# Kernel tuning notes

Measured on AMD Instinct MI355X. Metric: run time of the kernel, lower is better.

## Reference

```python
import jax, jax.numpy as jnp
import numpy as np

# Module constants (from init_kwargs)
D_MODEL = 2048
N_HEAD = 16
D_HEAD = D_MODEL // N_HEAD  # 128
CH = N_HEAD + D_HEAD        # 144
R_Q, R_K, R_V = 6, 2, 2
ROPE_BASE = 10000.0
B, T = 2, 2048


def _rotary(b, cache_len):
    # b: [B, T, R, dh]; rotary applied in factor space, positions offset by cache_len
    dh = b.shape[-1]
    inv_freq = (1.0 / ROPE_BASE) ** (jnp.arange(0, dh, 2, dtype=jnp.float32) / dh)
    t = jnp.arange(b.shape[1], dtype=jnp.float32) + cache_len
    freqs = t[:, None] * inv_freq[None, :]             # [T, dh/2]
    cos = jnp.cos(freqs)[None, :, None, :]
    sin = jnp.sin(freqs)[None, :, None, :]
    x1, x2 = jnp.split(b, 2, axis=-1)
    y1 = x1 * cos + x2 * sin
    y2 = -x1 * sin + x2 * cos
    return jnp.concatenate([y1, y2], axis=-1).astype(b.dtype)


def setup_inputs() -> dict:
    key = jax.random.key(0)
    k0, k1, k2, k3 = jax.random.split(key, 4)
    s = 1.0 / np.sqrt(D_MODEL)
    return {
        "x": jax.random.normal(k0, (B, T, D_MODEL), dtype=jnp.float32),
        "W_q": jax.random.normal(k1, (R_Q * CH, D_MODEL), dtype=jnp.float32) * s,
        "W_kv": jax.random.normal(k2, ((R_K + R_V) * CH, D_MODEL), dtype=jnp.float32) * s,
        "W_o": jax.random.normal(k3, (D_MODEL, D_MODEL), dtype=jnp.float32) * s,
    }


def reference(x, W_q, W_kv, W_o):
    Bx, Tx, D = x.shape
    nh, dh = N_HEAD, D_HEAD
    cache_len = 0  # empty cache, full prefill

    # Factorized Q projection: [B,T,r_Q,ch]
    abq = (x @ W_q.T).reshape(Bx, Tx, R_Q, CH)
    a_q, b_q = abq[..., :nh], abq[..., nh:]

    # Factorized KV projection, rotary in factor space on the b-part
    abkv = (x @ W_kv.T).reshape(Bx, Tx, R_K + R_V, CH)
    a_kv = abkv[..., :nh]
    b_kv = _rotary(abkv[..., nh:], cache_len)

    a_k, b_k = a_kv[:, :, :R_K], b_kv[:, :, :R_K]
    a_v, b_v = a_kv[:, :, R_K:], b_kv[:, :, R_K:]

    # Rank-r outer-product reconstruction: [B,T,nh,dh]
    q = jnp.einsum("btrh,btrd->bthd", a_q, b_q) * (1.0 / R_Q)
    k = jnp.einsum("btrh,btrd->bthd", a_k, b_k) * (1.0 / R_K)
    v = jnp.einsum("btrh,btrd->bthd", a_v, b_v) * (1.0 / R_V)

    # Causal attention (flex_attention default scale = 1/sqrt(dh))
    scale = 1.0 / np.sqrt(dh)
    scores = jnp.einsum("bqhd,bkhd->bhqk", q, k) * scale
    qi = jnp.arange(Tx)[:, None]
    ki = jnp.arange(Tx)[None, :]
    causal = ki <= qi + cache_len
    scores = jnp.where(causal[None, None], scores, jnp.finfo(scores.dtype).min)
    attn = jax.nn.softmax(scores, axis=-1)
    y = jnp.einsum("bhqk,bkhd->bqhd", attn, v).reshape(Bx, Tx, D)
    return y @ W_o.T
```

## Files before the change

kernel.cpp:

```cpp
#include <hip/hip_runtime.h>
#include <hip/hip_bf16.h>
#include <cstdint>
#include <cstddef>

#define T_SEQ   2048
#define BATCH   2
#define DMODEL  2048
#define NHEAD   16
#define DHEAD   128
#define CH      144
#define RQ      6
#define RKV     4
#define N1      1440
#define N1P     1536
#define MROWS   4096

typedef short bf16x8 __attribute__((ext_vector_type(8)));
typedef float f32x4  __attribute__((ext_vector_type(4)));

#if defined(__has_builtin)
#  if __has_builtin(__builtin_amdgcn_exp2f)
#    define EXP2(x) __builtin_amdgcn_exp2f(x)
#  else
#    define EXP2(x) exp2f(x)
#  endif
#else
#  define EXP2(x) exp2f(x)
#endif

__device__ __forceinline__ float bflo(unsigned u){ return __uint_as_float(u << 16); }
__device__ __forceinline__ float bfhi(unsigned u){ return __uint_as_float(u & 0xffff0000u); }
__device__ __forceinline__ unsigned short f2bf(float f){
  unsigned b = __float_as_uint(f);
  b += 0x7fffu + ((b >> 16) & 1u);
  return (unsigned short)(b >> 16);
}

__global__ void cast_f32_bf16(const float* __restrict__ src, unsigned short* __restrict__ dst, int n4){
  int i = blockIdx.x * blockDim.x + threadIdx.x;
  int stride = gridDim.x * blockDim.x;
  for (; i < n4; i += stride){
    float4 v = ((const float4*)src)[i];
    ushort4 o;
    o.x = f2bf(v.x); o.y = f2bf(v.y); o.z = f2bf(v.z); o.w = f2bf(v.w);
    ((ushort4*)dst)[i] = o;
  }
}

__global__ void zero_u16(unsigned short* __restrict__ dst, int n){
  int i = blockIdx.x * blockDim.x + threadIdx.x;
  if (i < n) dst[i] = 0;
}

#define GBK 32
__global__ __launch_bounds__(256) void gemm_bt(const unsigned short* __restrict__ A,
                                               const unsigned short* __restrict__ Bm,
                                               float* __restrict__ C,
                                               int M, int N, int K){
  __shared__ __align__(16) unsigned short As[128 * GBK];
  __shared__ __align__(16) unsigned short Bs[128 * GBK];
  const int tid  = threadIdx.x;
  const int lane = tid & 63;
  const int wv   = tid >> 6;
  const int m0   = blockIdx.y * 128;
  const int n0   = blockIdx.x * 128;
  const int wm   = wv >> 1, wn = wv & 1;

  f32x4 acc[4][4];
#pragma unroll
  for (int i = 0; i < 4; ++i)
#pragma unroll
    for (int j = 0; j < 4; ++j) acc[i][j] = (f32x4){0.f, 0.f, 0.f, 0.f};

  const int srow = lane >> 2;
  const int scol = (lane & 3) * 8;
  const int kq   = (lane >> 4) * 8;
  const int rA   = lane & 15;

  for (int kt = 0; kt < K; kt += GBK){
#pragma unroll
    for (int i = 0; i < 2; ++i){
      int j = wv * 2 + i;
      int r = j * 16 + srow;
      const unsigned short* ga = A  + (size_t)(m0 + r) * K + kt + scol;
      const unsigned short* gb = Bm + (size_t)(n0 + r) * K + kt + scol;
      __builtin_amdgcn_global_load_lds((const __attribute__((address_space(1))) void*)ga,
                                       (__attribute__((address_space(3))) void*)&As[j * 16 * GBK], 16, 0, 0);
      __builtin_amdgcn_global_load_lds((const __attribute__((address_space(1))) void*)gb,
                                       (__attribute__((address_space(3))) void*)&Bs[j * 16 * GBK], 16, 0, 0);
    }
    __syncthreads();

    bf16x8 af[4], bfv[4];
#pragma unroll
    for (int mi = 0; mi < 4; ++mi)
      af[mi] = *(const bf16x8*)&As[(wm * 64 + mi * 16 + rA) * GBK + kq];
#pragma unroll
    for (int ni = 0; ni < 4; ++ni)
      bfv[ni] = *(const bf16x8*)&Bs[(wn * 64 + ni * 16 + rA) * GBK + kq];
#pragma unroll
    for (int mi = 0; mi < 4; ++mi)
#pragma unroll
      for (int ni = 0; ni < 4; ++ni)
        acc[mi][ni] = __builtin_amdgcn_mfma_f32_16x16x32_bf16(af[mi], bfv[ni], acc[mi][ni], 0, 0, 0);
    __syncthreads();
  }

#pragma unroll
  for (int mi = 0; mi < 4; ++mi)
#pragma unroll
    for (int ni = 0; ni < 4; ++ni){
      int row = m0 + wm * 64 + mi * 16 + (lane >> 4) * 4;
      int col = n0 + wn * 64 + ni * 16 + (lane & 15);
#pragma unroll
      for (int r = 0; r < 4; ++r)
        C[(size_t)(row + r) * N + col] = acc[mi][ni][r];
    }
}

__global__ __launch_bounds__(256) void qkv_kernel(const float* __restrict__ ab,
                                                  unsigned short* __restrict__ qb,
                                                  unsigned short* __restrict__ kb,
                                                  unsigned short* __restrict__ vb){
  __shared__ float sab[N1];
  const int bt = blockIdx.x;
  const int b  = bt >> 11;
  const int t  = bt & 2047;
  const float* row = ab + (size_t)bt * N1P;
  for (int j = threadIdx.x; j < N1; j += 256) sab[j] = row[j];
  __syncthreads();

  {
    int r = threadIdx.x >> 6;
    int d = threadIdx.x & 63;
    float inv = exp2f(-(float)d * 0.20762050593046f);
    float fr  = (float)t * inv;
    float c = cosf(fr), s = sinf(fr);
    float x1 = sab[864 + r * CH + 16 + d];
    float x2 = sab[864 + r * CH + 16 + 64 + d];
    sab[864 + r * CH + 16 + d]      = x1 * c + x2 * s;
    sab[864 + r * CH + 16 + 64 + d] = x2 * c - x1 * s;
  }
  __syncthreads();

  const int h  = threadIdx.x >> 4;
  const int d0 = (threadIdx.x & 15) * 8;

  {
    float aq[RQ];
#pragma unroll
    for (int r = 0; r < RQ; ++r) aq[r] = sab[r * CH + h];
    union { unsigned short u16[8]; uint4 v; } pk;
#pragma unroll
    for (int j = 0; j < 8; ++j){
      float acc = 0.f;
#pragma unroll
      for (int r = 0; r < RQ; ++r) acc += aq[r] * sab[r * CH + 16 + d0 + j];
      pk.u16[j] = f2bf(acc * (1.f / 6.f));
    }
    *(uint4*)&qb[((size_t)(b * 16 + h) * T_SEQ + t) * DHEAD + d0] = pk.v;
  }
  {
    float a0 = sab[864 + 0 * CH + h], a1 = sab[864 + 1 * CH + h];
    union { unsigned short u16[8]; uint4 v; } pk;
#pragma unroll
    for (int j = 0; j < 8; ++j){
      float acc = a0 * sab[864 + 0 * CH + 16 + d0 + j] + a1 * sab[864 + 1 * CH + 16 + d0 + j];
      pk.u16[j] = f2bf(acc * 0.5f);
    }
    *(uint4*)&kb[((size_t)(b * 16 + h) * T_SEQ + t) * DHEAD + d0] = pk.v;
  }
  {
    float a0 = sab[864 + 2 * CH + h], a1 = sab[864 + 3 * CH + h];
    union { unsigned short u16[8]; uint4 v; } pk;
#pragma unroll
    for (int j = 0; j < 8; ++j){
      float acc = a0 * sab[864 + 2 * CH + 16 + d0 + j] + a1 * sab[864 + 3 * CH + 16 + d0 + j];
      pk.u16[j] = f2bf(acc * 0.5f);
    }
    *(uint4*)&vb[((size_t)(b * 16 + h) * T_SEQ + t) * DHEAD + d0] = pk.v;
  }
}

#define SCL 0.12752551286084110f
__global__ __launch_bounds__(512) void attn_mfma(const unsigned short* __restrict__ qg,
                                                 const unsigned short* __restrict__ kg,
                                                 const unsigned short* __restrict__ vg,
                                                 unsigned short* __restrict__ yg){
  __shared__ __align__(16) unsigned short Ks[2 * 64 * DHEAD];
  __shared__ __align__(16) unsigned short Vt[2 * DHEAD * 64];
  __shared__ __align__(16) unsigned short Ps[8 * 16 * 64];

  const int bi   = blockIdx.x;
  const int xcd  = bi & 7;
  const int slot = bi >> 3;
  const int bh   = (slot & 3) * 8 + xcd;
  const int pr   = slot >> 2;
  const int b    = bh >> 4;
  const int h    = bh & 15;
  const size_t base = (size_t)bh * T_SEQ * DHEAD;

  const int lane = threadIdx.x & 63;
  const int wv   = threadIdx.x >> 6;
  const int lo   = lane & 15;
  const int hi   = lane >> 4;

  for (int phase = 0; phase < 2; ++phase){
    const int qt    = phase ? pr : (15 - pr);
    const int q0    = qt * 128;
    const int qrow0 = q0 + wv * 16;

    bf16x8 qf[4];
#pragma unroll
    for (int ds = 0; ds < 4; ++ds){
      uint4 u = *(const uint4*)(qg + base + (size_t)(qrow0 + lo) * DHEAD + ds * 32 + hi * 8);
      unsigned w[4] = {u.x, u.y, u.z, u.w};
      union { unsigned short s[8]; bf16x8 v; } r;
#pragma unroll
      for (int q = 0; q < 4; ++q){
        r.s[2*q]   = f2bf(bflo(w[q]) * SCL);
        r.s[2*q+1] = f2bf(bfhi(w[q]) * SCL);
      }
      qf[ds] = r.v;
    }

    f32x4 o4[8];
#pragma unroll
    for (int dcb = 0; dcb < 8; ++dcb) o4[dcb] = (f32x4){0.f,0.f,0.f,0.f};
    float mrow[4], lrow[4];
#pragma unroll
    for (int r = 0; r < 4; ++r){ mrow[r] = -1e30f; lrow[r] = 0.f; }

    const int nt = 2 * qt + 2;

    {
#pragma unroll
      for (int i = 0; i < 2; ++i){
        int c    = (i * 8 + wv) * 64 + lane;
        int row  = c >> 4;
        int gcol = (c & 15) ^ (row & 7);
        const unsigned short* src = kg + base + (size_t)row * DHEAD + gcol * 8;
        __builtin_amdgcn_global_load_lds((const __attribute__((address_space(1))) void*)src,
                                         (__attribute__((address_space(3))) void*)&Ks[(i * 8 + wv) * 512], 16, 0, 0);
      }
      uint4 tv[2];
#pragma unroll
      for (int i = 0; i < 2; ++i)
        tv[i] = *(const uint4*)(vg + base + (size_t)lane * DHEAD + (i * 8 + wv) * 8);
#pragma unroll
      for (int i = 0; i < 2; ++i){
        int d0 = (i * 8 + wv) * 8;
        union { uint4 v; unsigned short u[8]; } t2; t2.v = tv[i];
#pragma unroll
        for (int j = 0; j < 8; ++j)
          Vt[(d0 + j) * 64 + (lane ^ (j << 3))] = t2.u[j];
      }
      __syncthreads();
    }

    for (int kt = 0; kt < nt; ++kt){
      const int cur = kt & 1;
      const int nxt = cur ^ 1;
      const bool pf = (kt + 1 < nt);
      uint4 tv[2];
      if (pf){
#pragma unroll
        for (int i = 0; i < 2; ++i){
          int c    = (i * 8 + wv) * 64 + lane;
          int row  = c >> 4;
          int gcol = (c & 15) ^ (row & 7);
          const unsigned short* src = kg + base + (size_t)((kt + 1) * 64 + row) * DHEAD + gcol * 8;
          __builtin_amdgcn_global_load_lds((const __attribute__((address_space(1))) void*)src,
                                           (__attribute__((address_space(3))) void*)&Ks[nxt * 8192 + (i * 8 + wv) * 512], 16, 0, 0);
        }
#pragma unroll
        for (int i = 0; i < 2; ++i)
          tv[i] = *(const uint4*)(vg + base + (size_t)((kt + 1) * 64 + lane) * DHEAD + (i * 8 + wv) * 8);
      }

      if (kt * 64 <= qrow0 + 15){
        const unsigned short* Kb = &Ks[cur * 8192];
        const unsigned short* Vb = &Vt[cur * 8192];

        f32x4 s4[4];
#pragma unroll
        for (int cb = 0; cb < 4; ++cb) s4[cb] = (f32x4){0.f,0.f,0.f,0.f};
        __builtin_amdgcn_s_setprio(1);
#pragma unroll
        for (int ds = 0; ds < 4; ++ds){
          bf16x8 kf[4];
#pragma unroll
          for (int cb = 0; cb < 4; ++cb){
            int kvr = cb * 16 + lo;
            kf[cb] = *(const bf16x8*)&Kb[kvr * DHEAD + ((ds * 32 + hi * 8) ^ ((kvr & 7) << 3))];
          }
#pragma unroll
          for (int cb = 0; cb < 4; ++cb)
            s4[cb] = __builtin_amdgcn_mfma_f32_16x16x32_bf16(qf[ds], kf[cb], s4[cb], 0, 0, 0);
        }
        __builtin_amdgcn_s_setprio(0);

        if (kt * 64 + 63 > qrow0){
#pragma unroll
          for (int cb = 0; cb < 4; ++cb)
#pragma unroll
            for (int r = 0; r < 4; ++r){
              int kv = kt * 64 + cb * 16 + lo;
              int q  = qrow0 + hi * 4 + r;
              if (kv > q) s4[cb][r] = -1e30f;
            }
        }

        float mx8[4];
#pragma unroll
        for (int r = 0; r < 4; ++r){
          float mx = fmaxf(fmaxf(s4[0][r], s4[1][r]), fmaxf(s4[2][r], s4[3][r]));
          mx = fmaxf(mx, __shfl_xor(mx, 1));
          mx = fmaxf(mx, __shfl_xor(mx, 2));
          mx = fmaxf(mx, __shfl_xor(mx, 4));
          mx = fmaxf(mx, __shfl_xor(mx, 8));
          mx8[r] = mx;
        }
        bool grow = false;
#pragma unroll
        for (int r = 0; r < 4; ++r) grow |= (mx8[r] > mrow[r] + 8.f);
        if (__any(grow)){
#pragma unroll
          for (int r = 0; r < 4; ++r){
            float mN = fmaxf(mrow[r], mx8[r]);
            float alpha = EXP2(mrow[r] - mN);
            mrow[r] = mN;
            lrow[r] *= alpha;
#pragma unroll
            for (int dcb = 0; dcb < 8; ++dcb) o4[dcb][r] *= alpha;
          }
        }
#pragma unroll
        for (int r = 0; r < 4; ++r){
          float m = mrow[r];
          float p0 = EXP2(s4[0][r] - m);
          float p1 = EXP2(s4[1][r] - m);
          float p2 = EXP2(s4[2][r] - m);
          float p3 = EXP2(s4[3][r] - m);
          float ps = p0 + p1 + p2 + p3;
          ps += __shfl_xor(ps, 1);
          ps += __shfl_xor(ps, 2);
          ps += __shfl_xor(ps, 4);
          ps += __shfl_xor(ps, 8);
          lrow[r] += ps;
          int qloc = hi * 4 + r;
          int sw   = ((qloc + (qloc >> 3)) & 7) << 3;
          int pb   = wv * 1024 + qloc * 64;
          Ps[pb + ((0 * 16 + lo) ^ sw)] = f2bf(p0);
          Ps[pb + ((1 * 16 + lo) ^ sw)] = f2bf(p1);
          Ps[pb + ((2 * 16 + lo) ^ sw)] = f2bf(p2);
          Ps[pb + ((3 * 16 + lo) ^ sw)] = f2bf(p3);
        }

        asm volatile("s_waitcnt lgkmcnt(0)" ::: "memory");

        __builtin_amdgcn_s_setprio(1);
#pragma unroll
        for (int ks = 0; ks < 2; ++ks){
          bf16x8 pa;
          {
            int qloc = lo;
            int sw   = ((qloc + (qloc >> 3)) & 7) << 3;
            pa = *(const bf16x8*)&Ps[wv * 1024 + qloc * 64 + ((ks * 32 + hi * 8) ^ sw)];
          }
#pragma unroll
          for (int dcb = 0; dcb < 8; ++dcb){
            int d = dcb * 16 + lo;
            bf16x8 vf = *(const bf16x8*)&Vb[d * 64 + ((ks * 32 + hi * 8) ^ ((d & 7) << 3))];
            o4[dcb] = __builtin_amdgcn_mfma_f32_16x16x32_bf16(pa, vf, o4[dcb], 0, 0, 0);
          }
        }
        __builtin_amdgcn_s_setprio(0);
      }

      if (pf){
#pragma unroll
        for (int i = 0; i < 2; ++i){
          int d0 = (i * 8 + wv) * 8;
          union { uint4 v; unsigned short u[8]; } t2; t2.v = tv[i];
#pragma unroll
          for (int j = 0; j < 8; ++j)
            Vt[nxt * 8192 + (d0 + j) * 64 + (lane ^ (j << 3))] = t2.u[j];
        }
      }
      __syncthreads();
    }

#pragma unroll
    for (int r = 0; r < 4; ++r){
      float inv = 1.f / lrow[r];
      int q = qrow0 + hi * 4 + r;
      size_t yb_ = ((size_t)(b * T_SEQ + q)) * DMODEL + h * DHEAD;
#pragma unroll
      for (int dcb = 0; dcb < 8; ++dcb)
        yg[yb_ + dcb * 16 + lo] = f2bf(o4[dcb][r] * inv);
    }
    __syncthreads();
  }
}

extern "C" void kernel_launch(void* const* d_in, const int* in_sizes, int n_in,
                              void* d_out, int out_size, void* d_ws, size_t ws_size,
                              hipStream_t stream) {
  const float* x   = (const float*)d_in[0];
  const float* Wq  = (const float*)d_in[1];
  const float* Wkv = (const float*)d_in[2];
  const float* Wo  = (const float*)d_in[3];
  float* out = (float*)d_out;

  char* ws = (char*)d_ws;
  size_t off = 0;
  auto alloc = [&](size_t bytes) -> void* {
    void* p = ws + off;
    off += (bytes + 255) & ~(size_t)255;
    return p;
  };
  unsigned short* xb = (unsigned short*)alloc((size_t)MROWS * DMODEL * 2);
  unsigned short* wc = (unsigned short*)alloc((size_t)N1P * DMODEL * 2);
  unsigned short* wo = (unsigned short*)alloc((size_t)DMODEL * DMODEL * 2);
  float*          abf = (float*)alloc((size_t)MROWS * N1P * 4);
  unsigned short* qb = (unsigned short*)alloc((size_t)MROWS * DMODEL * 2);
  unsigned short* kb = (unsigned short*)alloc((size_t)MROWS * DMODEL * 2);
  unsigned short* vb = (unsigned short*)alloc((size_t)MROWS * DMODEL * 2);
  unsigned short* yb = (unsigned short*)alloc((size_t)MROWS * DMODEL * 2);

  {
    int n4 = MROWS * DMODEL / 4;
    cast_f32_bf16<<<2048, 256, 0, stream>>>(x, xb, n4);
    n4 = RQ * CH * DMODEL / 4;
    cast_f32_bf16<<<1024, 256, 0, stream>>>(Wq, wc, n4);
    n4 = RKV * CH * DMODEL / 4;
    cast_f32_bf16<<<1024, 256, 0, stream>>>(Wkv, wc + (size_t)RQ * CH * DMODEL, n4);
    int npad = (N1P - N1) * DMODEL;
    zero_u16<<<(npad + 255) / 256, 256, 0, stream>>>(wc + (size_t)N1 * DMODEL, npad);
    n4 = DMODEL * DMODEL / 4;
    cast_f32_bf16<<<2048, 256, 0, stream>>>(Wo, wo, n4);
  }

  gemm_bt<<<dim3(N1P / 128, MROWS / 128), 256, 0, stream>>>(xb, wc, abf, MROWS, N1P, DMODEL);
  qkv_kernel<<<MROWS, 256, 0, stream>>>(abf, qb, kb, vb);
  attn_mfma<<<256, 512, 0, stream>>>(qb, kb, vb, yb);
  gemm_bt<<<dim3(DMODEL / 128, MROWS / 128), 256, 0, stream>>>(yb, wo, out, MROWS, DMODEL, DMODEL);
}
```

Baseline: 341.0 us.

## Process both causal query tiles concurrently in one 1024-thread attention block

The attention kernel previously ran two phases sequentially, one per query tile of a complementary causal pair. It now launches 1024 threads so waves 0-7 handle the long tile and waves 8-15 the short tile, sharing the same K/V loads from LDS. Shared tile loads are now spread over 16 waves. The Q softmax scale and log2e factor are folded into the qkv kernel, which removes the per-element rescale when Q is loaded. The cost is higher register pressure under launch_bounds(1024), and the short-tile waves sit idle for the later KV iterations while still taking part in the barriers.

```diff
diff --git a/kernel.cpp b/kernel.cpp
--- a/kernel.cpp
+++ b/kernel.cpp
@@ -118,6 +118,7 @@
     }
 }
 
+#define QSCL 0.021254252143473517f
 __global__ __launch_bounds__(256) void qkv_kernel(const float* __restrict__ ab,
                                                   unsigned short* __restrict__ qb,
                                                   unsigned short* __restrict__ kb,
@@ -156,7 +157,7 @@
       float acc = 0.f;
 #pragma unroll
       for (int r = 0; r < RQ; ++r) acc += aq[r] * sab[r * CH + 16 + d0 + j];
-      pk.u16[j] = f2bf(acc * (1.f / 6.f));
+      pk.u16[j] = f2bf(acc * QSCL);
     }
     *(uint4*)&qb[((size_t)(b * 16 + h) * T_SEQ + t) * DHEAD + d0] = pk.v;
   }
@@ -182,14 +183,13 @@
   }
 }
 
-#define SCL 0.12752551286084110f
-__global__ __launch_bounds__(512) void attn_mfma(const unsigned short* __restrict__ qg,
-                                                 const unsigned short* __restrict__ kg,
-                                                 const unsigned short* __restrict__ vg,
-                                                 unsigned short* __restrict__ yg){
+__global__ __launch_bounds__(1024) void attn_mfma(const unsigned short* __restrict__ qg,
+                                                  const unsigned short* __restrict__ kg,
+                                                  const unsigned short* __restrict__ vg,
+                                                  unsigned short* __restrict__ yg){
   __shared__ __align__(16) unsigned short Ks[2 * 64 * DHEAD];
   __shared__ __align__(16) unsigned short Vt[2 * DHEAD * 64];
-  __shared__ __align__(16) unsigned short Ps[8 * 16 * 64];
+  __shared__ __align__(16) unsigned short Ps[16 * 16 * 64];
 
   const int bi   = blockIdx.x;
   const int xcd  = bi & 7;
@@ -202,205 +202,173 @@
 
   const int lane = threadIdx.x & 63;
   const int wv   = threadIdx.x >> 6;
+  const int wl   = wv & 7;
   const int lo   = lane & 15;
   const int hi   = lane >> 4;
 
-  for (int phase = 0; phase < 2; ++phase){
-    const int qt    = phase ? pr : (15 - pr);
-    const int q0    = qt * 128;
-    const int qrow0 = q0 + wv * 16;
-
-    bf16x8 qf[4];
-#pragma unroll
-    for (int ds = 0; ds < 4; ++ds){
-      uint4 u = *(const uint4*)(qg + base + (size_t)(qrow0 + lo) * DHEAD + ds * 32 + hi * 8);
-      unsigned w[4] = {u.x, u.y, u.z, u.w};
-      union { unsigned short s[8]; bf16x8 v; } r;
-#pragma unroll
-      for (int q = 0; q < 4; ++q){
-        r.s[2*q]   = f2bf(bflo(w[q]) * SCL);
-        r.s[2*q+1] = f2bf(bfhi(w[q]) * SCL);
-      }
-      qf[ds] = r.v;
-    }
-
-    f32x4 o4[8];
-#pragma unroll
-    for (int dcb = 0; dcb < 8; ++dcb) o4[dcb] = (f32x4){0.f,0.f,0.f,0.f};
-    float mrow[4], lrow[4];
-#pragma unroll
-    for (int r = 0; r < 4; ++r){ mrow[r] = -1e30f; lrow[r] = 0.f; }
-
-    const int nt = 2 * qt + 2;
-
-    {
-#pragma unroll
-      for (int i = 0; i < 2; ++i){
-        int c    = (i * 8 + wv) * 64 + lane;
-        int row  = c >> 4;
-        int gcol = (c & 15) ^ (row & 7);
-        const unsigned short* src = kg + base + (size_t)row * DHEAD + gcol * 8;
-        __builtin_amdgcn_global_load_lds((const __attribute__((address_space(1))) void*)src,
-                                         (__attribute__((address_space(3))) void*)&Ks[(i * 8 + wv) * 512], 16, 0, 0);
-      }
-      uint4 tv[2];
-#pragma unroll
-      for (int i = 0; i < 2; ++i)
-        tv[i] = *(const uint4*)(vg + base + (size_t)lane * DHEAD + (i * 8 + wv) * 8);
-#pragma unroll
-      for (int i = 0; i < 2; ++i){
-        int d0 = (i * 8 + wv) * 8;
-        union { uint4 v; unsigned short u[8]; } t2; t2.v = tv[i];
-#pragma unroll
-        for (int j = 0; j < 8; ++j)
-          Vt[(d0 + j) * 64 + (lane ^ (j << 3))] = t2.u[j];
-      }
-      __syncthreads();
-    }
-
-    for (int kt = 0; kt < nt; ++kt){
-      const int cur = kt & 1;
-      const int nxt = cur ^ 1;
-      const bool pf = (kt + 1 < nt);
-      uint4 tv[2];
-      if (pf){
-#pragma unroll
-        for (int i = 0; i < 2; ++i){
-          int c    = (i * 8 + wv) * 64 + lane;
-          int row  = c >> 4;
-          int gcol = (c & 15) ^ (row & 7);
-          const unsigned short* src = kg + base + (size_t)((kt + 1) * 64 + row) * DHEAD + gcol * 8;
-          __builtin_amdgcn_global_load_lds((const __attribute__((address_space(1))) void*)src,
-                                           (__attribute__((address_space(3))) void*)&Ks[nxt * 8192 + (i * 8 + wv) * 512], 16, 0, 0);
+  const int qt    = (wv < 8) ? (15 - pr) : pr;
+  const int qrow0 = qt * 128 + wl * 16;
+  const int nt    = 2 * (15 - pr) + 2;
+
+  bf16x8 qf[4];
+#pragma unroll
+  for (int ds = 0; ds < 4; ++ds)
+    qf[ds] = *(const bf16x8*)(qg + base + (size_t)(qrow0 + lo) * DHEAD + ds * 32 + hi * 8);
+
+  f32x4 o4[8];
+#pragma unroll
+  for (int dcb = 0; dcb < 8; ++dcb) o4[dcb] = (f32x4){0.f,0.f,0.f,0.f};
+  float mrow[4], lrow[4];
+#pragma unroll
+  for (int r = 0; r < 4; ++r){ mrow[r] = -1e30f; lrow[r] = 0.f; }
+
+  {
+    int c    = threadIdx.x;
+    int row  = c >> 4;
+    int gcol = (c & 15) ^ (row & 7);
+    const unsigned short* src = kg + base + (size_t)row * DHEAD + gcol * 8;
+    __builtin_amdgcn_global_load_lds((const __attribute__((address_space(1))) void*)src,
+                                     (__attribute__((address_space(3))) void*)&Ks[wv * 512], 16, 0, 0);
+    uint4 tv = *(const uint4*)(vg + base + (size_t)lane * DHEAD + wv * 8);
+    union { uint4 v; unsigned short u[8]; } t2; t2.v = tv;
+#pragma unroll
+    for (int j = 0; j < 8; ++j)
+      Vt[(wv * 8 + j) * 64 + (lane ^ (j << 3))] = t2.u[j];
+    __syncthreads();
+  }
+
+  for (int kt = 0; kt < nt; ++kt){
+    const int cur = kt & 1;
+    const int nxt = cur ^ 1;
+    const bool pf = (kt + 1 < nt);
+    uint4 tv;
+    if (pf){
+      int c    = threadIdx.x;
+      int row  = c >> 4;
+      int gcol = (c & 15) ^ (row & 7);
+      const unsigned short* src = kg + base + (size_t)((kt + 1) * 64 + row) * DHEAD + gcol * 8;
+      __builtin_amdgcn_global_load_lds((const __attribute__((address_space(1))) void*)src,
+                                       (__attribute__((address_space(3))) void*)&Ks[nxt * 8192 + wv * 512], 16, 0, 0);
+      tv = *(const uint4*)(vg + base + (size_t)((kt + 1) * 64 + lane) * DHEAD + wv * 8);
+    }
+
+    if (kt * 64 <= qrow0 + 15){
+      const unsigned short* Kb = &Ks[cur * 8192];
+      const unsigned short* Vb = &Vt[cur * 8192];
+
+      f32x4 s4[4];
+#pragma unroll
+      for (int cb = 0; cb < 4; ++cb) s4[cb] = (f32x4){0.f,0.f,0.f,0.f};
+      __builtin_amdgcn_s_setprio(1);
+#pragma unroll
+      for (int ds = 0; ds < 4; ++ds){
+        bf16x8 kf[4];
+#pragma unroll
+        for (int cb = 0; cb < 4; ++cb){
+          int kvr = cb * 16 + lo;
+          kf[cb] = *(const bf16x8*)&Kb[kvr * DHEAD + ((ds * 32 + hi * 8) ^ ((kvr & 7) << 3))];
         }
 #pragma unroll
-        for (int i = 0; i < 2; ++i)
-          tv[i] = *(const uint4*)(vg + base + (size_t)((kt + 1) * 64 + lane) * DHEAD + (i * 8 + wv) * 8);
-      }
-
-      if (kt * 64 <= qrow0 + 15){
-        const unsigned short* Kb = &Ks[cur * 8192];
-        const unsigned short* Vb = &Vt[cur * 8192];
-
-        f32x4 s4[4];
-#pragma unroll
-        for (int cb = 0; cb < 4; ++cb) s4[cb] = (f32x4){0.f,0.f,0.f,0.f};
-        __builtin_amdgcn_s_setprio(1);
-#pragma unroll
-        for (int ds = 0; ds < 4; ++ds){
-          bf16x8 kf[4];
-#pragma unroll
-          for (int cb = 0; cb < 4; ++cb){
-            int kvr = cb * 16 + lo;
-            kf[cb] = *(const bf16x8*)&Kb[kvr * DHEAD + ((ds * 32 + hi * 8) ^ ((kvr & 7) << 3))];
+        for (int cb = 0; cb < 4; ++cb)
+          s4[cb] = __builtin_amdgcn_mfma_f32_16x16x32_bf16(qf[ds], kf[cb], s4[cb], 0, 0, 0);
+      }
+      __builtin_amdgcn_s_setprio(0);
+
+      if (kt * 64 + 63 > qrow0){
+#pragma unroll
+        for (int cb = 0; cb < 4; ++cb)
+#pragma unroll
+          for (int r = 0; r < 4; ++r){
+            int kv = kt * 64 + cb * 16 + lo;
+            int q  = qrow0 + hi * 4 + r;
+            if (kv > q) s4[cb][r] = -1e30f;
           }
-#pragma unroll
-          for (int cb = 0; cb < 4; ++cb)
-            s4[cb] = __builtin_amdgcn_mfma_f32_16x16x32_bf16(qf[ds], kf[cb], s4[cb], 0, 0, 0);
+      }
+
+      float mx8[4];
+#pragma unroll
+      for (int r = 0; r < 4; ++r){
+        float mx = fmaxf(fmaxf(s4[0][r], s4[1][r]), fmaxf(s4[2][r], s4[3][r]));
+        mx = fmaxf(mx, __shfl_xor(mx, 1));
+        mx = fmaxf(mx, __shfl_xor(mx, 2));
+        mx = fmaxf(mx, __shfl_xor(mx, 4));
+        mx = fmaxf(mx, __shfl_xor(mx, 8));
+        mx8[r] = mx;
+      }
+      bool grow = false;
+#pragma unroll
+      for (int r = 0; r < 4; ++r) grow |= (mx8[r] > mrow[r] + 8.f);
+      if (__any(grow)){
+#pragma unroll
+        for (int r = 0; r < 4; ++r){
+          float mN = fmaxf(mrow[r], mx8[r]);
+          float alpha = EXP2(mrow[r] - mN);
+          mrow[r] = mN;
+          lrow[r] *= alpha;
+#pragma unroll
+          for (int dcb = 0; dcb < 8; ++dcb) o4[dcb][r] *= alpha;
         }
-        __builtin_amdgcn_s_setprio(0);
-
-        if (kt * 64 + 63 > qrow0){
-#pragma unroll
-          for (int cb = 0; cb < 4; ++cb)
-#pragma unroll
-            for (int r = 0; r < 4; ++r){
-              int kv = kt * 64 + cb * 16 + lo;
-              int q  = qrow0 + hi * 4 + r;
-              if (kv > q) s4[cb][r] = -1e30f;
-            }
+      }
+#pragma unroll
+      for (int r = 0; r < 4; ++r){
+        float m = mrow[r];
+        float p0 = EXP2(s4[0][r] - m);
+        float p1 = EXP2(s4[1][r] - m);
+        float p2 = EXP2(s4[2][r] - m);
+        float p3 = EXP2(s4[3][r] - m);
+        float ps = p0 + p1 + p2 + p3;
+        ps += __shfl_xor(ps, 1);
+        ps += __shfl_xor(ps, 2);
+        ps += __shfl_xor(ps, 4);
+        ps += __shfl_xor(ps, 8);
+        lrow[r] += ps;
+        int qloc = hi * 4 + r;
+        int sw   = ((qloc + (qloc >> 3)) & 7) << 3;
+        int pb   = wv * 1024 + qloc * 64;
+        Ps[pb + ((0 * 16 + lo) ^ sw)] = f2bf(p0);
+        Ps[pb + ((1 * 16 + lo) ^ sw)] = f2bf(p1);
+        Ps[pb + ((2 * 16 + lo) ^ sw)] = f2bf(p2);
+        Ps[pb + ((3 * 16 + lo) ^ sw)] = f2bf(p3);
+      }
+
+      asm volatile("s_waitcnt lgkmcnt(0)" ::: "memory");
+
+      __builtin_amdgcn_s_setprio(1);
+#pragma unroll
+      for (int ks = 0; ks < 2; ++ks){
+        bf16x8 pa;
+        {
+          int qloc = lo;
+          int sw   = ((qloc + (qloc >> 3)) & 7) << 3;
+          pa = *(const bf16x8*)&Ps[wv * 1024 + qloc * 64 + ((ks * 32 + hi * 8) ^ sw)];
         }
-
-        float mx8[4];
-#pragma unroll
-        for (int r = 0; r < 4; ++r){
-          float mx = fmaxf(fmaxf(s4[0][r], s4[1][r]), fmaxf(s4[2][r], s4[3][r]));
-          mx = fmaxf(mx, __shfl_xor(mx, 1));
-          mx = fmaxf(mx, __shfl_xor(mx, 2));
-          mx = fmaxf(mx, __shfl_xor(mx, 4));
-          mx = fmaxf(mx, __shfl_xor(mx, 8));
-          mx8[r] = mx;
+#pragma unroll
+        for (int dcb = 0; dcb < 8; ++dcb){
+          int d = dcb * 16 + lo;
+          bf16x8 vf = *(const bf16x8*)&Vb[d * 64 + ((ks * 32 + hi * 8) ^ ((d & 7) << 3))];
+          o4[dcb] = __builtin_amdgcn_mfma_f32_16x16x32_bf16(pa, vf, o4[dcb], 0, 0, 0);
         }
-        bool grow = false;
-#pragma unroll
-        for (int r = 0; r < 4; ++r) grow |= (mx8[r] > mrow[r] + 8.f);
-        if (__any(grow)){
-#pragma unroll
-          for (int r = 0; r < 4; ++r){
-            float mN = fmaxf(mrow[r], mx8[r]);
-            float alpha = EXP2(mrow[r] - mN);
-            mrow[r] = mN;
-            lrow[r] *= alpha;
-#pragma unroll
-            for (int dcb = 0; dcb < 8; ++dcb) o4[dcb][r] *= alpha;
-          }
-        }
-#pragma unroll
-        for (int r = 0; r < 4; ++r){
-          float m = mrow[r];
-          float p0 = EXP2(s4[0][r] - m);
-          float p1 = EXP2(s4[1][r] - m);
-          float p2 = EXP2(s4[2][r] - m);
-          float p3 = EXP2(s4[3][r] - m);
-          float ps = p0 + p1 + p2 + p3;
-          ps += __shfl_xor(ps, 1);
-          ps += __shfl_xor(ps, 2);
-          ps += __shfl_xor(ps, 4);
-          ps += __shfl_xor(ps, 8);
-          lrow[r] += ps;
-          int qloc = hi * 4 + r;
-          int sw   = ((qloc + (qloc >> 3)) & 7) << 3;
-          int pb   = wv * 1024 + qloc * 64;
-          Ps[pb + ((0 * 16 + lo) ^ sw)] = f2bf(p0);
-          Ps[pb + ((1 * 16 + lo) ^ sw)] = f2bf(p1);
-          Ps[pb + ((2 * 16 + lo) ^ sw)] = f2bf(p2);
-          Ps[pb + ((3 * 16 + lo) ^ sw)] = f2bf(p3);
-        }
-
-        asm volatile("s_waitcnt lgkmcnt(0)" ::: "memory");
-
-        __builtin_amdgcn_s_setprio(1);
-#pragma unroll
-        for (int ks = 0; ks < 2; ++ks){
-          bf16x8 pa;
-          {
-            int qloc = lo;
-            int sw   = ((qloc + (qloc >> 3)) & 7) << 3;
-            pa = *(const bf16x8*)&Ps[wv * 1024 + qloc * 64 + ((ks * 32 + hi * 8) ^ sw)];
-          }
-#pragma unroll
-          for (int dcb = 0; dcb < 8; ++dcb){
-            int d = dcb * 16 + lo;
-            bf16x8 vf = *(const bf16x8*)&Vb[d * 64 + ((ks * 32 + hi * 8) ^ ((d & 7) << 3))];
-            o4[dcb] = __builtin_amdgcn_mfma_f32_16x16x32_bf16(pa, vf, o4[dcb], 0, 0, 0);
-          }
-        }
-        __builtin_amdgcn_s_setprio(0);
-      }
-
-      if (pf){
-#pragma unroll
-        for (int i = 0; i < 2; ++i){
-          int d0 = (i * 8 + wv) * 8;
-          union { uint4 v; unsigned short u[8]; } t2; t2.v = tv[i];
-#pragma unroll
-          for (int j = 0; j < 8; ++j)
-            Vt[nxt * 8192 + (d0 + j) * 64 + (lane ^ (j << 3))] = t2.u[j];
-        }
-      }
-      __syncthreads();
-    }
-
-#pragma unroll
-    for (int r = 0; r < 4; ++r){
-      float inv = 1.f / lrow[r];
-      int q = qrow0 + hi * 4 + r;
-      size_t yb_ = ((size_t)(b * T_SEQ + q)) * DMODEL + h * DHEAD;
-#pragma unroll
-      for (int dcb = 0; dcb < 8; ++dcb)
-        yg[yb_ + dcb * 16 + lo] = f2bf(o4[dcb][r] * inv);
+      }
+      __builtin_amdgcn_s_setprio(0);
+    }
+
+    if (pf){
+      union { uint4 v; unsigned short u[8]; } t2; t2.v = tv;
+#pragma unroll
+      for (int j = 0; j < 8; ++j)
+        Vt[nxt * 8192 + (wv * 8 + j) * 64 + (lane ^ (j << 3))] = t2.u[j];
     }
     __syncthreads();
+  }
+
+#pragma unroll
+  for (int r = 0; r < 4; ++r){
+    float inv = 1.f / lrow[r];
+    int q = qrow0 + hi * 4 + r;
+    size_t yb_ = ((size_t)(b * T_SEQ + q)) * DMODEL + h * DHEAD;
+#pragma unroll
+    for (int dcb = 0; dcb < 8; ++dcb)
+      yg[yb_ + dcb * 16 + lo] = f2bf(o4[dcb][r] * inv);
   }
 }
 
@@ -444,6 +412,6 @@
 
   gemm_bt<<<dim3(N1P / 128, MROWS / 128), 256, 0, stream>>>(xb, wc, abf, MROWS, N1P, DMODEL);
   qkv_kernel<<<MROWS, 256, 0, stream>>>(abf, qb, kb, vb);
-  attn_mfma<<<256, 512, 0, stream>>>(qb, kb, vb, yb);
+  attn_mfma<<<256, 1024, 0, stream>>>(qb, kb, vb, yb);
   gemm_bt<<<dim3(DMODEL / 128, MROWS / 128), 256, 0, stream>>>(yb, wo, out, MROWS, DMODEL, DMODEL);
 }
```

After: 375.3 us. 10.0% more time.

## Transpose QK^T MFMA so each lane owns one query row; fold Q scale into projection

Applied to the files above, without the earlier changes.

The S=QK^T MFMA operands are swapped so the score tile comes out transposed, with each lane holding one query row across 16 keys. Row max and row sum then need only two cross-lane shuffles instead of four per row, and P is written to LDS with packed 8-byte stores into a padded 72-wide buffer. The softmax scale is folded into the Q reconstruction scale in the QKV kernel, so Q no longer needs an unpack-rescale-repack step in attention. The cost is extra shuffles to broadcast alpha and the final row sum to the O layout, plus slightly more LDS for the padded P buffer.

```diff
diff --git a/kernel.cpp b/kernel.cpp
--- a/kernel.cpp
+++ b/kernel.cpp
@@ -118,6 +118,7 @@
     }
 }
 
+#define QSCL 0.021254252143473517f
 __global__ __launch_bounds__(256) void qkv_kernel(const float* __restrict__ ab,
                                                   unsigned short* __restrict__ qb,
                                                   unsigned short* __restrict__ kb,
@@ -156,7 +157,7 @@
       float acc = 0.f;
 #pragma unroll
       for (int r = 0; r < RQ; ++r) acc += aq[r] * sab[r * CH + 16 + d0 + j];
-      pk.u16[j] = f2bf(acc * (1.f / 6.f));
+      pk.u16[j] = f2bf(acc * QSCL);
     }
     *(uint4*)&qb[((size_t)(b * 16 + h) * T_SEQ + t) * DHEAD + d0] = pk.v;
   }
@@ -182,14 +183,13 @@
   }
 }
 
-#define SCL 0.12752551286084110f
 __global__ __launch_bounds__(512) void attn_mfma(const unsigned short* __restrict__ qg,
                                                  const unsigned short* __restrict__ kg,
                                                  const unsigned short* __restrict__ vg,
                                                  unsigned short* __restrict__ yg){
   __shared__ __align__(16) unsigned short Ks[2 * 64 * DHEAD];
   __shared__ __align__(16) unsigned short Vt[2 * DHEAD * 64];
-  __shared__ __align__(16) unsigned short Ps[8 * 16 * 64];
+  __shared__ __align__(16) unsigned short Ps[8 * 16 * 72];
 
   const int bi   = blockIdx.x;
   const int xcd  = bi & 7;
@@ -207,29 +207,17 @@
 
   for (int phase = 0; phase < 2; ++phase){
     const int qt    = phase ? pr : (15 - pr);
-    const int q0    = qt * 128;
-    const int qrow0 = q0 + wv * 16;
+    const int qrow0 = qt * 128 + wv * 16;
 
     bf16x8 qf[4];
 #pragma unroll
-    for (int ds = 0; ds < 4; ++ds){
-      uint4 u = *(const uint4*)(qg + base + (size_t)(qrow0 + lo) * DHEAD + ds * 32 + hi * 8);
-      unsigned w[4] = {u.x, u.y, u.z, u.w};
-      union { unsigned short s[8]; bf16x8 v; } r;
-#pragma unroll
-      for (int q = 0; q < 4; ++q){
-        r.s[2*q]   = f2bf(bflo(w[q]) * SCL);
-        r.s[2*q+1] = f2bf(bfhi(w[q]) * SCL);
-      }
-      qf[ds] = r.v;
-    }
+    for (int ds = 0; ds < 4; ++ds)
+      qf[ds] = *(const bf16x8*)(qg + base + (size_t)(qrow0 + lo) * DHEAD + ds * 32 + hi * 8);
 
     f32x4 o4[8];
 #pragma unroll
     for (int dcb = 0; dcb < 8; ++dcb) o4[dcb] = (f32x4){0.f,0.f,0.f,0.f};
-    float mrow[4], lrow[4];
-#pragma unroll
-    for (int r = 0; r < 4; ++r){ mrow[r] = -1e30f; lrow[r] = 0.f; }
+    float mrow = -1e30f, lsum = 0.f;
 
     const int nt = 2 * qt + 2;
 
@@ -296,65 +284,63 @@
           }
 #pragma unroll
           for (int cb = 0; cb < 4; ++cb)
-            s4[cb] = __builtin_amdgcn_mfma_f32_16x16x32_bf16(qf[ds], kf[cb], s4[cb], 0, 0, 0);
+            s4[cb] = __builtin_amdgcn_mfma_f32_16x16x32_bf16(kf[cb], qf[ds], s4[cb], 0, 0, 0);
         }
         __builtin_amdgcn_s_setprio(0);
 
+        const int qrow = qrow0 + lo;
         if (kt * 64 + 63 > qrow0){
 #pragma unroll
           for (int cb = 0; cb < 4; ++cb)
 #pragma unroll
             for (int r = 0; r < 4; ++r){
-              int kv = kt * 64 + cb * 16 + lo;
-              int q  = qrow0 + hi * 4 + r;
-              if (kv > q) s4[cb][r] = -1e30f;
+              int kv = kt * 64 + cb * 16 + hi * 4 + r;
+              if (kv > qrow) s4[cb][r] = -1e30f;
             }
         }
 
-        float mx8[4];
-#pragma unroll
-        for (int r = 0; r < 4; ++r){
-          float mx = fmaxf(fmaxf(s4[0][r], s4[1][r]), fmaxf(s4[2][r], s4[3][r]));
-          mx = fmaxf(mx, __shfl_xor(mx, 1));
-          mx = fmaxf(mx, __shfl_xor(mx, 2));
-          mx = fmaxf(mx, __shfl_xor(mx, 4));
-          mx = fmaxf(mx, __shfl_xor(mx, 8));
-          mx8[r] = mx;
-        }
-        bool grow = false;
-#pragma unroll
-        for (int r = 0; r < 4; ++r) grow |= (mx8[r] > mrow[r] + 8.f);
-        if (__any(grow)){
+        float mx = s4[0][0];
+#pragma unroll
+        for (int cb = 0; cb < 4; ++cb)
+#pragma unroll
+          for (int r = 0; r < 4; ++r) mx = fmaxf(mx, s4[cb][r]);
+        mx = fmaxf(mx, __shfl_xor(mx, 16));
+        mx = fmaxf(mx, __shfl_xor(mx, 32));
+
+        if (__any(mx > mrow + 8.f)){
+          float mN = fmaxf(mrow, mx);
+          float alpha = EXP2(mrow - mN);
+          mrow = mN;
+          lsum *= alpha;
 #pragma unroll
           for (int r = 0; r < 4; ++r){
-            float mN = fmaxf(mrow[r], mx8[r]);
-            float alpha = EXP2(mrow[r] - mN);
-            mrow[r] = mN;
-            lrow[r] *= alpha;
-#pragma unroll
-            for (int dcb = 0; dcb < 8; ++dcb) o4[dcb][r] *= alpha;
+            float ar = __shfl(alpha, hi * 4 + r);
+#pragma unroll
+            for (int dcb = 0; dcb < 8; ++dcb) o4[dcb][r] *= ar;
           }
         }
-#pragma unroll
-        for (int r = 0; r < 4; ++r){
-          float m = mrow[r];
-          float p0 = EXP2(s4[0][r] - m);
-          float p1 = EXP2(s4[1][r] - m);
-          float p2 = EXP2(s4[2][r] - m);
-          float p3 = EXP2(s4[3][r] - m);
-          float ps = p0 + p1 + p2 + p3;
-          ps += __shfl_xor(ps, 1);
-          ps += __shfl_xor(ps, 2);
-          ps += __shfl_xor(ps, 4);
-          ps += __shfl_xor(ps, 8);
-          lrow[r] += ps;
-          int qloc = hi * 4 + r;
-          int sw   = ((qloc + (qloc >> 3)) & 7) << 3;
-          int pb   = wv * 1024 + qloc * 64;
-          Ps[pb + ((0 * 16 + lo) ^ sw)] = f2bf(p0);
-          Ps[pb + ((1 * 16 + lo) ^ sw)] = f2bf(p1);
-          Ps[pb + ((2 * 16 + lo) ^ sw)] = f2bf(p2);
-          Ps[pb + ((3 * 16 + lo) ^ sw)] = f2bf(p3);
+
+        float p[4][4];
+        float psum = 0.f;
+#pragma unroll
+        for (int cb = 0; cb < 4; ++cb)
+#pragma unroll
+          for (int r = 0; r < 4; ++r){
+            float v = EXP2(s4[cb][r] - mrow);
+            p[cb][r] = v;
+            psum += v;
+          }
+        psum += __shfl_xor(psum, 16);
+        psum += __shfl_xor(psum, 32);
+        lsum += psum;
+
+#pragma unroll
+        for (int cb = 0; cb < 4; ++cb){
+          unsigned u0 = (unsigned)f2bf(p[cb][0]) | ((unsigned)f2bf(p[cb][1]) << 16);
+          unsigned u1 = (unsigned)f2bf(p[cb][2]) | ((unsigned)f2bf(p[cb][3]) << 16);
+          uint2 w; w.x = u0; w.y = u1;
+          int off = (wv * 16 + lo) * 72 + ((cb ^ (lo & 3)) * 16) + hi * 4;
+          *(uint2*)&Ps[off] = w;
         }
 
         asm volatile("s_waitcnt lgkmcnt(0)" ::: "memory");
@@ -364,9 +350,9 @@
         for (int ks = 0; ks < 2; ++ks){
           bf16x8 pa;
           {
-            int qloc = lo;
-            int sw   = ((qloc + (qloc >> 3)) & 7) << 3;
-            pa = *(const bf16x8*)&Ps[wv * 1024 + qloc * 64 + ((ks * 32 + hi * 8) ^ sw)];
+            int g = (2 * ks + (hi >> 1)) ^ (lo & 3);
+            int off = (wv * 16 + lo) * 72 + g * 16 + (hi & 1) * 8;
+            pa = *(const bf16x8*)&Ps[off];
           }
 #pragma unroll
           for (int dcb = 0; dcb < 8; ++dcb){
@@ -393,7 +379,8 @@
 
 #pragma unroll
     for (int r = 0; r < 4; ++r){
-      float inv = 1.f / lrow[r];
+      float lr  = __shfl(lsum, hi * 4 + r);
+      float inv = 1.f / lr;
       int q = qrow0 + hi * 4 + r;
       size_t yb_ = ((size_t)(b * T_SEQ + q)) * DMODEL + h * DHEAD;
 #pragma unroll
```

Result: faster. 322.3 us (-5.5%).
